# Kernel optimization log

Measured on AMD Instinct MI355X. Metric: run time of the kernel, lower is better.

## Reference

```python
import jax, jax.numpy as jnp
import numpy as np
from jax import lax

D_MODEL, D_INNER, D_CONV, DT_RANK, D_STATE = 1024, 2048, 4, 64, 16
B_SZ, L = 1, 2048
EPS = 1e-5


def setup_inputs() -> dict:
    key = jax.random.key(0)
    ks = jax.random.split(key, 10)
    s = 0.02
    return {
        "x": jax.random.normal(ks[0], (B_SZ, L, D_MODEL), dtype=jnp.float32),
        "W_in": jax.random.normal(ks[1], (2 * D_INNER, D_MODEL), dtype=jnp.float32) * s,
        "conv_w": jax.random.normal(ks[2], (D_INNER, D_CONV), dtype=jnp.float32) * 0.1,
        "conv_b": jnp.zeros((D_INNER,), dtype=jnp.float32),
        "W_xproj": jax.random.normal(ks[3], (DT_RANK + 2 * D_STATE, D_INNER), dtype=jnp.float32) * s,
        "W_dt": jax.random.normal(ks[4], (D_INNER, DT_RANK), dtype=jnp.float32) * s,
        "b_dt": jnp.zeros((D_INNER,), dtype=jnp.float32),
        "A_log": jnp.broadcast_to(jnp.log(jnp.arange(1, D_STATE + 1, dtype=jnp.float32)), (D_INNER, D_STATE)).copy(),
        "D": jnp.ones((D_INNER,), dtype=jnp.float32),
        "W_out": jax.random.normal(ks[5], (D_MODEL, D_INNER), dtype=jnp.float32) * s,
        "norm_w": jnp.ones((D_MODEL,), dtype=jnp.float32),
    }


def _mamba_block(xn, W_in, conv_w, conv_b, W_xproj, W_dt, b_dt, A_log, D, W_out):
    b, l, _ = xn.shape
    # in_proj -> split into x branch and gate (res) branch
    xz = jnp.einsum("bld,ed->ble", xn, W_in)  # (b, l, 2*d_inner)
    xc, res = jnp.split(xz, 2, axis=-1)
    # depthwise causal conv1d over time (padding=d_conv-1, trimmed to l)
    xp = jnp.pad(xc, ((0, 0), (D_CONV - 1, 0), (0, 0)))
    conv = conv_b
    acc = jnp.zeros_like(xc)
    for k in range(D_CONV):
        acc = acc + xp[:, k:k + l, :] * conv_w[:, k]
    xs = jax.nn.silu(acc + conv_b)  # (b, l, d_inner)
    # x_proj -> delta (low-rank), B, C
    dbc = jnp.einsum("bld,ed->ble", xs, W_xproj)
    dt, Bm, Cm = jnp.split(dbc, [DT_RANK, DT_RANK + D_STATE], axis=-1)
    delta = jax.nn.softplus(jnp.einsum("blr,dr->bld", dt, W_dt) + b_dt)  # (b,l,d_inner)
    A = -jnp.exp(A_log)  # (d_inner, d_state)
    # discretize
    deltaA = jnp.exp(jnp.einsum("bld,dn->bldn", delta, A))
    dBu = jnp.einsum("bld,bln,bld->bldn", delta, Bm, xs)
    # selective scan over time
    def step(h, inp):
        dA_t, dBu_t, C_t = inp
        h = dA_t * h + dBu_t                      # (b, d_inner, d_state)
        y_t = jnp.einsum("bdn,bn->bd", h, C_t)
        return h, y_t
    h0 = jnp.zeros((b, D_INNER, D_STATE), dtype=xs.dtype)
    _, ys = lax.scan(step, h0, (deltaA.transpose(1, 0, 2, 3), dBu.transpose(1, 0, 2, 3), Cm.transpose(1, 0, 2)))
    y = ys.transpose(1, 0, 2) + xs * D  # (b, l, d_inner)
    y = y * jax.nn.silu(res)            # gate
    return jnp.einsum("bld,ed->ble", y, W_out)


def reference(x, W_in, conv_w, conv_b, W_xproj, W_dt, b_dt, A_log, D, W_out, norm_w):
    # RMSNorm
    xn = x * jax.lax.rsqrt(jnp.mean(x * x, axis=-1, keepdims=True) + EPS) * norm_w
    # Mamba mixer + residual
    return _mamba_block(xn, W_in, conv_w, conv_b, W_xproj, W_dt, b_dt, A_log, D, W_out) + x
```

## Files before the change

### kernel.cpp

```cpp
#include <hip/hip_runtime.h>
#include <hip/hip_bf16.h>

#define D_MODEL 1024
#define D_INNER 2048
#define DT_RANK 64
#define D_STATE 16
#define LSEQ    2048
#define CHUNK   32
#define NCHUNK  (LSEQ / CHUNK)
#define DN      (D_INNER * D_STATE)
#define KSPL_O  4
#define KSPL_X  16

typedef __attribute__((ext_vector_type(8))) short  short8;
typedef __attribute__((ext_vector_type(4))) float  float4v;
typedef __hip_bfloat16 bf16;

static __device__ __forceinline__ float b2f(bf16 v) { return __bfloat162float(v); }
static __device__ __forceinline__ bf16  f2b(float v) { return __float2bfloat16(v); }

#define GLOAD_LDS16(g, l)                                                          \
    __builtin_amdgcn_global_load_lds((const __attribute__((address_space(1))) void*)(g), \
                                     (__attribute__((address_space(3))) void*)(l), 16, 0, 0)

#define N1 (2 * D_INNER * D_MODEL)
#define N2 (D_MODEL * D_INNER)
#define N3 (96 * D_INNER)
#define N4 (D_INNER * DT_RANK)
__global__ __launch_bounds__(256)
void cast_all(const float* __restrict__ w_in, const float* __restrict__ w_out,
              const float* __restrict__ w_xp, const float* __restrict__ w_dt,
              bf16* __restrict__ o_in, bf16* __restrict__ o_out,
              bf16* __restrict__ o_xp, bf16* __restrict__ o_dt) {
    int i4 = blockIdx.x * 256 + threadIdx.x;
    const float* src; bf16* dst; int base;
    if (i4 < N1 / 4)                { src = w_in;  dst = o_in;  base = 0; }
    else if (i4 < (N1 + N2) / 4)    { src = w_out; dst = o_out; base = N1 / 4; }
    else if (i4 < (N1+N2+N3) / 4)   { src = w_xp;  dst = o_xp;  base = (N1+N2) / 4; }
    else if (i4 < (N1+N2+N3+N4)/4)  { src = w_dt;  dst = o_dt;  base = (N1+N2+N3) / 4; }
    else return;
    int j = i4 - base;
    float4v v = ((const float4v*)src)[j];
    bf16* o = dst + j * 4;
    o[0] = f2b(v[0]); o[1] = f2b(v[1]); o[2] = f2b(v[2]); o[3] = f2b(v[3]);
}

__global__ void rms_kernel(const float* __restrict__ x, const float* __restrict__ nw,
                           bf16* __restrict__ xn) {
    int l = blockIdx.x, t = threadIdx.x;
    float4v v = ((const float4v*)(x + (size_t)l * D_MODEL))[t];
    float ssq = v[0]*v[0] + v[1]*v[1] + v[2]*v[2] + v[3]*v[3];
    for (int o = 32; o > 0; o >>= 1) ssq += __shfl_down(ssq, o);
    __shared__ float part[4];
    int lane = t & 63, wid = t >> 6;
    if (lane == 0) part[wid] = ssq;
    __syncthreads();
    float tot = part[0] + part[1] + part[2] + part[3];
    float sc = rsqrtf(tot * (1.0f / D_MODEL) + 1e-5f);
    float4v nv = ((const float4v*)nw)[t];
    bf16* op = xn + (size_t)l * D_MODEL + t * 4;
    op[0] = f2b(v[0] * sc * nv[0]);
    op[1] = f2b(v[1] * sc * nv[1]);
    op[2] = f2b(v[2] * sc * nv[2]);
    op[3] = f2b(v[3] * sc * nv[3]);
}

template <int MODE>
__global__ __launch_bounds__(256)
void gemm_fast(const bf16* __restrict__ Ab, const bf16* __restrict__ Bb,
               int M, int N, int K, int kLen,
               float* __restrict__ outF, bf16* __restrict__ outB,
               const float* __restrict__ bias) {
    __shared__ short As[2][128 * 32];
    __shared__ short Bs[2][128 * 32];
    const short* Ap = (const short*)Ab;
    const short* Bp = (const short*)Bb;

    int t = threadIdx.x;
    int lane = t & 63, wid = t >> 6;
    int mBase = blockIdx.y * 128, nBase = blockIdx.x * 128;
    int kBase = blockIdx.z * kLen;
    int wm = (wid >> 1) * 64, wn = (wid & 1) * 64;
    int lr = lane & 15, quad = lane >> 4;

    int srow = 32 * wid + (lane >> 2);
    int cg = (lane & 3) ^ ((lane >> 3) & 3);
    const short* gA0 = Ap + (size_t)(mBase + srow) * K + cg * 8;
    const short* gA1 = gA0 + (size_t)16 * K;
    const short* gB0 = Bp + (size_t)(nBase + srow) * K + cg * 8;
    const short* gB1 = gB0 + (size_t)16 * K;

    float4v acc[4][4] = {};
    int sw = (lr >> 1) & 3;

    GLOAD_LDS16(gA0 + kBase, &As[0][(32 * wid) * 32]);
    GLOAD_LDS16(gA1 + kBase, &As[0][(32 * wid + 16) * 32]);
    GLOAD_LDS16(gB0 + kBase, &Bs[0][(32 * wid) * 32]);
    GLOAD_LDS16(gB1 + kBase, &Bs[0][(32 * wid + 16) * 32]);

    int p = 0;
    for (int kt = kBase; kt < kBase + kLen; kt += 32, p ^= 1) {
        __syncthreads();
        if (kt + 32 < kBase + kLen) {
            int kn = kt + 32, q = p ^ 1;
            GLOAD_LDS16(gA0 + kn, &As[q][(32 * wid) * 32]);
            GLOAD_LDS16(gA1 + kn, &As[q][(32 * wid + 16) * 32]);
            GLOAD_LDS16(gB0 + kn, &Bs[q][(32 * wid) * 32]);
            GLOAD_LDS16(gB1 + kn, &Bs[q][(32 * wid + 16) * 32]);
        }
        short8 af[4], bfr[4];
        #pragma unroll
        for (int i = 0; i < 4; ++i)
            af[i] = *(const short8*)&As[p][(wm + i * 16 + lr) * 32 + ((quad ^ sw) * 8)];
        #pragma unroll
        for (int j = 0; j < 4; ++j)
            bfr[j] = *(const short8*)&Bs[p][(wn + j * 16 + lr) * 32 + ((quad ^ sw) * 8)];
        #pragma unroll
        for (int i = 0; i < 4; ++i)
            #pragma unroll
            for (int j = 0; j < 4; ++j)
                acc[i][j] = __builtin_amdgcn_mfma_f32_16x16x32_bf16(af[i], bfr[j], acc[i][j], 0, 0, 0);
    }

    #pragma unroll
    for (int i = 0; i < 4; ++i) {
        #pragma unroll
        for (int j = 0; j < 4; ++j) {
            #pragma unroll
            for (int r = 0; r < 4; ++r) {
                int gm = mBase + wm + i * 16 + quad * 4 + r;
                int gn = nBase + wn + j * 16 + lr;
                float v = acc[i][j][r];
                if (MODE == 0) {
                    outB[(size_t)gm * N + gn] = f2b(v);
                } else if (MODE == 2) {
                    v += bias[gn];
                    v = (v > 20.0f) ? v : log1pf(__expf(v));
                    outB[(size_t)gm * N + gn] = f2b(v);
                } else {
                    outF[((size_t)blockIdx.z * M + gm) * N + gn] = v;
                }
            }
        }
    }
}

__global__ __launch_bounds__(128)
void reduce_xproj(const float* __restrict__ part, float* __restrict__ dbc,
                  bf16* __restrict__ dtb) {
    int m = blockIdx.x, j = threadIdx.x;
    if (j >= 96) return;
    float v = 0.0f;
    #pragma unroll
    for (int z = 0; z < KSPL_X; ++z)
        v += part[((size_t)z * LSEQ + m) * 128 + j];
    dbc[(size_t)m * 96 + j] = v;
    if (j < DT_RANK) dtb[(size_t)m * DT_RANK + j] = f2b(v);
}

__global__ __launch_bounds__(256)
void reduce_out(const float* __restrict__ part, const float* __restrict__ x,
                float* __restrict__ out) {
    int i = blockIdx.x * 256 + threadIdx.x;
    const int MN4 = LSEQ * D_MODEL / 4;
    float4v a = ((const float4v*)part)[i];
    #pragma unroll
    for (int z = 1; z < KSPL_O; ++z) {
        float4v b = ((const float4v*)part)[(size_t)z * MN4 + i];
        a[0] += b[0]; a[1] += b[1]; a[2] += b[2]; a[3] += b[3];
    }
    float4v xv = ((const float4v*)x)[i];
    a[0] += xv[0]; a[1] += xv[1]; a[2] += xv[2]; a[3] += xv[3];
    ((float4v*)out)[i] = a;
}

__global__ void conv_kernel(const bf16* __restrict__ xz, const float* __restrict__ cw,
                            const float* __restrict__ cb, bf16* __restrict__ xsb) {
    int idx = blockIdx.x * 256 + threadIdx.x;
    int c = idx & (D_INNER - 1);
    int l = idx >> 11;
    float w0 = cw[c * 4 + 0], w1 = cw[c * 4 + 1];
    float w2 = cw[c * 4 + 2], w3 = cw[c * 4 + 3];
    float acc = cb[c];
    const bf16* col = xz + c;
    if (l >= 3) acc += b2f(col[(size_t)(l - 3) * (2 * D_INNER)]) * w0;
    if (l >= 2) acc += b2f(col[(size_t)(l - 2) * (2 * D_INNER)]) * w1;
    if (l >= 1) acc += b2f(col[(size_t)(l - 1) * (2 * D_INNER)]) * w2;
    acc += b2f(col[(size_t)l * (2 * D_INNER)]) * w3;
    float s = acc * (1.0f / (1.0f + __expf(-acc)));
    xsb[idx] = f2b(s);
}

template <int PASS>
__global__ __launch_bounds__(256)
void scan2(const bf16* __restrict__ delta, const bf16* __restrict__ xsb,
           const float* __restrict__ dbc, const bf16* __restrict__ xz,
           const float* __restrict__ A_log, const float* __restrict__ Dw,
           const float* __restrict__ Hinit,
           float* __restrict__ P, float* __restrict__ S, bf16* __restrict__ yg) {
    __shared__ float bc[CHUNK][32];
    int t = threadIdx.x;
    int d = blockIdx.x * 256 + t;
    int c = blockIdx.y;
    int l0 = c * CHUNK;

    {
        int row = t >> 3, col = (t & 7) * 4;
        *(float4v*)&bc[row][col] = *(const float4v*)&dbc[(size_t)(l0 + row) * 96 + 64 + col];
    }
    __syncthreads();

    float A[16], h[16], pr[16];
    #pragma unroll
    for (int n = 0; n < 16; ++n) A[n] = -__expf(A_log[(size_t)d * 16 + n]);
    if (PASS == 0) {
        #pragma unroll
        for (int n = 0; n < 16; ++n) { h[n] = 0.0f; pr[n] = 1.0f; }
    } else {
        #pragma unroll
        for (int n = 0; n < 16; n += 4)
            *(float4v*)&h[n] = *(const float4v*)&Hinit[(size_t)c * DN + (size_t)d * 16 + n];
    }
    float Dd = (PASS == 1) ? Dw[d] : 0.0f;

    for (int i = 0; i < CHUNK; ++i) {
        int l = l0 + i;
        float dv = b2f(delta[(size_t)l * D_INNER + d]);
        float xv = b2f(xsb[(size_t)l * D_INNER + d]);
        float u = dv * xv;
        float Bv[16];
        #pragma unroll
        for (int n = 0; n < 16; n += 4) *(float4v*)&Bv[n] = *(const float4v*)&bc[i][n];
        #pragma unroll
        for (int n = 0; n < 16; ++n) {
            float a = __expf(dv * A[n]);
            h[n] = fmaf(a, h[n], Bv[n] * u);
            if (PASS == 0) pr[n] *= a;
        }
        if (PASS == 1) {
            float Cv[16];
            #pragma unroll
            for (int n = 0; n < 16; n += 4) *(float4v*)&Cv[n] = *(const float4v*)&bc[i][16 + n];
            float y = xv * Dd;
            #pragma unroll
            for (int n = 0; n < 16; ++n) y = fmaf(h[n], Cv[n], y);
            float r = b2f(xz[(size_t)l * (2 * D_INNER) + D_INNER + d]);
            float g = r * (1.0f / (1.0f + __expf(-r)));
            yg[(size_t)l * D_INNER + d] = f2b(y * g);
        }
    }
    if (PASS == 0) {
        #pragma unroll
        for (int n = 0; n < 16; n += 4) {
            *(float4v*)&P[(size_t)c * DN + (size_t)d * 16 + n] = *(float4v*)&pr[n];
            *(float4v*)&S[(size_t)c * DN + (size_t)d * 16 + n] = *(float4v*)&h[n];
        }
    }
}

__global__ __launch_bounds__(256)
void scan_mid(const float* __restrict__ P, const float* __restrict__ S,
              float* __restrict__ Hinit) {
    int idx = blockIdx.x * 256 + threadIdx.x;
    float h = 0.0f;
    for (int c0 = 0; c0 < NCHUNK; c0 += 8) {
        float p[8], s[8];
        #pragma unroll
        for (int j = 0; j < 8; ++j) {
            p[j] = P[(size_t)(c0 + j) * DN + idx];
            s[j] = S[(size_t)(c0 + j) * DN + idx];
        }
        #pragma unroll
        for (int j = 0; j < 8; ++j) {
            Hinit[(size_t)(c0 + j) * DN + idx] = h;
            h = fmaf(p[j], h, s[j]);
        }
    }
}

extern "C" void kernel_launch(void* const* d_in, const int* in_sizes, int n_in,
                              void* d_out, int out_size, void* d_ws, size_t ws_size,
                              hipStream_t stream) {
    const float* x       = (const float*)d_in[0];
    const float* W_in    = (const float*)d_in[1];
    const float* conv_w  = (const float*)d_in[2];
    const float* conv_b  = (const float*)d_in[3];
    const float* W_xproj = (const float*)d_in[4];
    const float* W_dt    = (const float*)d_in[5];
    const float* b_dt    = (const float*)d_in[6];
    const float* A_log   = (const float*)d_in[7];
    const float* Dw      = (const float*)d_in[8];
    const float* W_out   = (const float*)d_in[9];
    const float* norm_w  = (const float*)d_in[10];

    char* w = (char*)d_ws;
    bf16* W_in_b    = (bf16*)w; w += (size_t)2 * D_INNER * D_MODEL * 2;
    bf16* W_out_b   = (bf16*)w; w += (size_t)D_MODEL * D_INNER * 2;
    bf16* W_xproj_b = (bf16*)w; w += (size_t)128 * D_INNER * 2;
    bf16* W_dt_b    = (bf16*)w; w += (size_t)D_INNER * DT_RANK * 2;
    char* reuse0 = w;
    bf16* xn        = (bf16*)w; w += (size_t)LSEQ * D_MODEL * 2;
    bf16* xz        = (bf16*)w; w += (size_t)LSEQ * 2 * D_INNER * 2;
    bf16* xsb       = (bf16*)w; w += (size_t)LSEQ * D_INNER * 2;
    bf16* delta     = (bf16*)w; w += (size_t)LSEQ * D_INNER * 2;
    float* dbc      = (float*)w; w += (size_t)LSEQ * 96 * 4;
    bf16* dtb       = (bf16*)w; w += (size_t)LSEQ * DT_RANK * 2;
    bf16* yg        = (bf16*)w; w += (size_t)LSEQ * D_INNER * 2;
    float* Pbuf     = (float*)w; w += (size_t)NCHUNK * DN * 4;
    float* Sbuf     = (float*)w; w += (size_t)NCHUNK * DN * 4;
    float* Hinit    = (float*)w; w += (size_t)NCHUNK * DN * 4;
    float* xp_part  = (float*)w; w += (size_t)KSPL_X * LSEQ * 128 * 4;
    float* out_part = (float*)reuse0;

    cast_all<<<(N1 + N2 + N3 + N4) / 4 / 256, 256, 0, stream>>>(
        W_in, W_out, W_xproj, W_dt, W_in_b, W_out_b, W_xproj_b, W_dt_b);

    rms_kernel<<<LSEQ, 256, 0, stream>>>(x, norm_w, xn);

    gemm_fast<0><<<dim3(4096 / 128, 2048 / 128, 1), 256, 0, stream>>>(
        xn, W_in_b, 2048, 4096, 1024, 1024, nullptr, xz, nullptr);

    conv_kernel<<<(LSEQ * D_INNER) / 256, 256, 0, stream>>>(xz, conv_w, conv_b, xsb);

    gemm_fast<4><<<dim3(1, 2048 / 128, KSPL_X), 256, 0, stream>>>(
        xsb, W_xproj_b, 2048, 128, 2048, 2048 / KSPL_X, xp_part, nullptr, nullptr);
    reduce_xproj<<<LSEQ, 128, 0, stream>>>(xp_part, dbc, dtb);

    gemm_fast<2><<<dim3(2048 / 128, 2048 / 128, 1), 256, 0, stream>>>(
        dtb, W_dt_b, 2048, 2048, 64, 64, nullptr, delta, b_dt);

    dim3 sgrid(D_INNER / 256, NCHUNK);
    scan2<0><<<sgrid, 256, 0, stream>>>(delta, xsb, dbc, xz, A_log, Dw,
                                        nullptr, Pbuf, Sbuf, nullptr);
    scan_mid<<<DN / 256, 256, 0, stream>>>(Pbuf, Sbuf, Hinit);
    scan2<1><<<sgrid, 256, 0, stream>>>(delta, xsb, dbc, xz, A_log, Dw,
                                        Hinit, nullptr, nullptr, yg);

    gemm_fast<4><<<dim3(1024 / 128, 2048 / 128, KSPL_O), 256, 0, stream>>>(
        yg, W_out_b, 2048, 1024, 2048, 2048 / KSPL_O, out_part, nullptr, nullptr);
    reduce_out<<<LSEQ * D_MODEL / 4 / 256, 256, 0, stream>>>(out_part, x, (float*)d_out);
}
```

Baseline: 265.8 us.

## Double GEMM K-tile to 64, fuse RMSNorm with weight cast, 4-step conv

The bf16 MFMA GEMM now stages 64-wide K tiles in LDS, with an 8-way XOR swizzle and two MFMA sub-steps per barrier. This halves the number of barriers and loop iterations per output tile, at the cost of twice the LDS per block. RMSNorm and the weight fp32-to-bf16 cast are merged into one launch to remove a kernel boundary. The depthwise conv kernel now computes four consecutive timesteps per thread, reusing overlapping input loads across the window.

After: 253.1 us. 4.8% less time.

```diff
diff --git a/kernel.cpp b/kernel.cpp
--- a/kernel.cpp
+++ b/kernel.cpp
@@ -27,52 +27,55 @@
 #define N2 (D_MODEL * D_INNER)
 #define N3 (96 * D_INNER)
 #define N4 (D_INNER * DT_RANK)
-__global__ __launch_bounds__(256)
-void cast_all(const float* __restrict__ w_in, const float* __restrict__ w_out,
-              const float* __restrict__ w_xp, const float* __restrict__ w_dt,
-              bf16* __restrict__ o_in, bf16* __restrict__ o_out,
-              bf16* __restrict__ o_xp, bf16* __restrict__ o_dt) {
-    int i4 = blockIdx.x * 256 + threadIdx.x;
+#define NCAST4 ((N1 + N2 + N3 + N4) / 4)
+__global__ __launch_bounds__(256)
+void prep_kernel(const float* __restrict__ x, const float* __restrict__ nw,
+                 bf16* __restrict__ xn,
+                 const float* __restrict__ w_in, const float* __restrict__ w_out,
+                 const float* __restrict__ w_xp, const float* __restrict__ w_dt,
+                 bf16* __restrict__ o_in, bf16* __restrict__ o_out,
+                 bf16* __restrict__ o_xp, bf16* __restrict__ o_dt) {
+    int t = threadIdx.x;
+    if (blockIdx.x < LSEQ) {
+        int l = blockIdx.x;
+        float4v v = ((const float4v*)(x + (size_t)l * D_MODEL))[t];
+        float ssq = v[0]*v[0] + v[1]*v[1] + v[2]*v[2] + v[3]*v[3];
+        for (int o = 32; o > 0; o >>= 1) ssq += __shfl_down(ssq, o);
+        __shared__ float part[4];
+        int lane = t & 63, wid = t >> 6;
+        if (lane == 0) part[wid] = ssq;
+        __syncthreads();
+        float tot = part[0] + part[1] + part[2] + part[3];
+        float sc = rsqrtf(tot * (1.0f / D_MODEL) + 1e-5f);
+        float4v nv = ((const float4v*)nw)[t];
+        bf16* op = xn + (size_t)l * D_MODEL + t * 4;
+        op[0] = f2b(v[0] * sc * nv[0]);
+        op[1] = f2b(v[1] * sc * nv[1]);
+        op[2] = f2b(v[2] * sc * nv[2]);
+        op[3] = f2b(v[3] * sc * nv[3]);
+        return;
+    }
+    int i4 = (blockIdx.x - LSEQ) * 256 + t;
+    if (i4 >= NCAST4) return;
     const float* src; bf16* dst; int base;
     if (i4 < N1 / 4)                { src = w_in;  dst = o_in;  base = 0; }
     else if (i4 < (N1 + N2) / 4)    { src = w_out; dst = o_out; base = N1 / 4; }
     else if (i4 < (N1+N2+N3) / 4)   { src = w_xp;  dst = o_xp;  base = (N1+N2) / 4; }
-    else if (i4 < (N1+N2+N3+N4)/4)  { src = w_dt;  dst = o_dt;  base = (N1+N2+N3) / 4; }
-    else return;
+    else                            { src = w_dt;  dst = o_dt;  base = (N1+N2+N3) / 4; }
     int j = i4 - base;
     float4v v = ((const float4v*)src)[j];
     bf16* o = dst + j * 4;
     o[0] = f2b(v[0]); o[1] = f2b(v[1]); o[2] = f2b(v[2]); o[3] = f2b(v[3]);
 }
 
-__global__ void rms_kernel(const float* __restrict__ x, const float* __restrict__ nw,
-                           bf16* __restrict__ xn) {
-    int l = blockIdx.x, t = threadIdx.x;
-    float4v v = ((const float4v*)(x + (size_t)l * D_MODEL))[t];
-    float ssq = v[0]*v[0] + v[1]*v[1] + v[2]*v[2] + v[3]*v[3];
-    for (int o = 32; o > 0; o >>= 1) ssq += __shfl_down(ssq, o);
-    __shared__ float part[4];
-    int lane = t & 63, wid = t >> 6;
-    if (lane == 0) part[wid] = ssq;
-    __syncthreads();
-    float tot = part[0] + part[1] + part[2] + part[3];
-    float sc = rsqrtf(tot * (1.0f / D_MODEL) + 1e-5f);
-    float4v nv = ((const float4v*)nw)[t];
-    bf16* op = xn + (size_t)l * D_MODEL + t * 4;
-    op[0] = f2b(v[0] * sc * nv[0]);
-    op[1] = f2b(v[1] * sc * nv[1]);
-    op[2] = f2b(v[2] * sc * nv[2]);
-    op[3] = f2b(v[3] * sc * nv[3]);
-}
-
 template <int MODE>
 __global__ __launch_bounds__(256)
 void gemm_fast(const bf16* __restrict__ Ab, const bf16* __restrict__ Bb,
                int M, int N, int K, int kLen,
                float* __restrict__ outF, bf16* __restrict__ outB,
                const float* __restrict__ bias) {
-    __shared__ short As[2][128 * 32];
-    __shared__ short Bs[2][128 * 32];
+    __shared__ short As[2][128 * 64];
+    __shared__ short Bs[2][128 * 64];
     const short* Ap = (const short*)Ab;
     const short* Bp = (const short*)Bb;
 
@@ -83,43 +86,49 @@
     int wm = (wid >> 1) * 64, wn = (wid & 1) * 64;
     int lr = lane & 15, quad = lane >> 4;
 
-    int srow = 32 * wid + (lane >> 2);
-    int cg = (lane & 3) ^ ((lane >> 3) & 3);
-    const short* gA0 = Ap + (size_t)(mBase + srow) * K + cg * 8;
-    const short* gA1 = gA0 + (size_t)16 * K;
-    const short* gB0 = Bp + (size_t)(nBase + srow) * K + cg * 8;
-    const short* gB1 = gB0 + (size_t)16 * K;
+    int srow = 32 * wid + (lane >> 3);
+    int cg = (lane & 7) ^ (lane >> 3);
+    const short* gA = Ap + (size_t)(mBase + srow) * K + cg * 8;
+    const short* gB = Bp + (size_t)(nBase + srow) * K + cg * 8;
 
     float4v acc[4][4] = {};
-    int sw = (lr >> 1) & 3;
-
-    GLOAD_LDS16(gA0 + kBase, &As[0][(32 * wid) * 32]);
-    GLOAD_LDS16(gA1 + kBase, &As[0][(32 * wid + 16) * 32]);
-    GLOAD_LDS16(gB0 + kBase, &Bs[0][(32 * wid) * 32]);
-    GLOAD_LDS16(gB1 + kBase, &Bs[0][(32 * wid + 16) * 32]);
+
+    #pragma unroll
+    for (int g = 0; g < 4; ++g) {
+        GLOAD_LDS16(gA + (size_t)g * 8 * K + kBase, &As[0][(32 * wid + g * 8) * 64]);
+        GLOAD_LDS16(gB + (size_t)g * 8 * K + kBase, &Bs[0][(32 * wid + g * 8) * 64]);
+    }
 
     int p = 0;
-    for (int kt = kBase; kt < kBase + kLen; kt += 32, p ^= 1) {
+    for (int kt = kBase; kt < kBase + kLen; kt += 64, p ^= 1) {
         __syncthreads();
-        if (kt + 32 < kBase + kLen) {
-            int kn = kt + 32, q = p ^ 1;
-            GLOAD_LDS16(gA0 + kn, &As[q][(32 * wid) * 32]);
-            GLOAD_LDS16(gA1 + kn, &As[q][(32 * wid + 16) * 32]);
-            GLOAD_LDS16(gB0 + kn, &Bs[q][(32 * wid) * 32]);
-            GLOAD_LDS16(gB1 + kn, &Bs[q][(32 * wid + 16) * 32]);
-        }
-        short8 af[4], bfr[4];
-        #pragma unroll
-        for (int i = 0; i < 4; ++i)
-            af[i] = *(const short8*)&As[p][(wm + i * 16 + lr) * 32 + ((quad ^ sw) * 8)];
-        #pragma unroll
-        for (int j = 0; j < 4; ++j)
-            bfr[j] = *(const short8*)&Bs[p][(wn + j * 16 + lr) * 32 + ((quad ^ sw) * 8)];
-        #pragma unroll
-        for (int i = 0; i < 4; ++i)
-            #pragma unroll
-            for (int j = 0; j < 4; ++j)
-                acc[i][j] = __builtin_amdgcn_mfma_f32_16x16x32_bf16(af[i], bfr[j], acc[i][j], 0, 0, 0);
+        if (kt + 64 < kBase + kLen) {
+            int kn = kt + 64, q = p ^ 1;
+            #pragma unroll
+            for (int g = 0; g < 4; ++g) {
+                GLOAD_LDS16(gA + (size_t)g * 8 * K + kn, &As[q][(32 * wid + g * 8) * 64]);
+                GLOAD_LDS16(gB + (size_t)g * 8 * K + kn, &Bs[q][(32 * wid + g * 8) * 64]);
+            }
+        }
+        #pragma unroll
+        for (int s = 0; s < 2; ++s) {
+            short8 af[4], bfr[4];
+            #pragma unroll
+            for (int i = 0; i < 4; ++i) {
+                int row = wm + i * 16 + lr;
+                af[i] = *(const short8*)&As[p][row * 64 + (((s * 4 + quad) ^ (lr & 7)) * 8)];
+            }
+            #pragma unroll
+            for (int j = 0; j < 4; ++j) {
+                int row = wn + j * 16 + lr;
+                bfr[j] = *(const short8*)&Bs[p][row * 64 + (((s * 4 + quad) ^ (lr & 7)) * 8)];
+            }
+            #pragma unroll
+            for (int i = 0; i < 4; ++i)
+                #pragma unroll
+                for (int j = 0; j < 4; ++j)
+                    acc[i][j] = __builtin_amdgcn_mfma_f32_16x16x32_bf16(af[i], bfr[j], acc[i][j], 0, 0, 0);
+        }
     }
 
     #pragma unroll
@@ -178,17 +187,23 @@
                             const float* __restrict__ cb, bf16* __restrict__ xsb) {
     int idx = blockIdx.x * 256 + threadIdx.x;
     int c = idx & (D_INNER - 1);
-    int l = idx >> 11;
+    int l0 = (idx >> 11) * 4;
     float w0 = cw[c * 4 + 0], w1 = cw[c * 4 + 1];
     float w2 = cw[c * 4 + 2], w3 = cw[c * 4 + 3];
-    float acc = cb[c];
+    float b = cb[c];
     const bf16* col = xz + c;
-    if (l >= 3) acc += b2f(col[(size_t)(l - 3) * (2 * D_INNER)]) * w0;
-    if (l >= 2) acc += b2f(col[(size_t)(l - 2) * (2 * D_INNER)]) * w1;
-    if (l >= 1) acc += b2f(col[(size_t)(l - 1) * (2 * D_INNER)]) * w2;
-    acc += b2f(col[(size_t)l * (2 * D_INNER)]) * w3;
-    float s = acc * (1.0f / (1.0f + __expf(-acc)));
-    xsb[idx] = f2b(s);
+    float v[7];
+    #pragma unroll
+    for (int j = 0; j < 7; ++j) {
+        int l = l0 - 3 + j;
+        v[j] = (l >= 0) ? b2f(col[(size_t)l * (2 * D_INNER)]) : 0.0f;
+    }
+    #pragma unroll
+    for (int j = 0; j < 4; ++j) {
+        float acc = b + v[j] * w0 + v[j + 1] * w1 + v[j + 2] * w2 + v[j + 3] * w3;
+        float s = acc * (1.0f / (1.0f + __expf(-acc)));
+        xsb[(size_t)(l0 + j) * D_INNER + c] = f2b(s);
+    }
 }
 
 template <int PASS>
@@ -312,15 +327,13 @@
     float* xp_part  = (float*)w; w += (size_t)KSPL_X * LSEQ * 128 * 4;
     float* out_part = (float*)reuse0;
 
-    cast_all<<<(N1 + N2 + N3 + N4) / 4 / 256, 256, 0, stream>>>(
-        W_in, W_out, W_xproj, W_dt, W_in_b, W_out_b, W_xproj_b, W_dt_b);
-
-    rms_kernel<<<LSEQ, 256, 0, stream>>>(x, norm_w, xn);
+    prep_kernel<<<LSEQ + (NCAST4 + 255) / 256, 256, 0, stream>>>(
+        x, norm_w, xn, W_in, W_out, W_xproj, W_dt, W_in_b, W_out_b, W_xproj_b, W_dt_b);
 
     gemm_fast<0><<<dim3(4096 / 128, 2048 / 128, 1), 256, 0, stream>>>(
         xn, W_in_b, 2048, 4096, 1024, 1024, nullptr, xz, nullptr);
 
-    conv_kernel<<<(LSEQ * D_INNER) / 256, 256, 0, stream>>>(xz, conv_w, conv_b, xsb);
+    conv_kernel<<<(LSEQ / 4 * D_INNER) / 256, 256, 0, stream>>>(xz, conv_w, conv_b, xsb);
 
     gemm_fast<4><<<dim3(1, 2048 / 128, KSPL_X), 256, 0, stream>>>(
         xsb, W_xproj_b, 2048, 128, 2048, 2048 / KSPL_X, xp_part, nullptr, nullptr);
```
